# Kernel tuning notes

Hardware: AMD Instinct MI355X
Metric: run time of the kernel (lower is better)

Reference implementation:

```python
import jax, jax.numpy as jnp
import numpy as np

D_MODEL = 256
N_LAYER = 8
N_HEAD = 8
D_K = D_MODEL // N_HEAD  # 32
D_FF = 4 * D_MODEL
VOCAB = 5
NUM_BUCKETS = 64
MAX_DIST = 256
L = 768
B = 1
EPS = 1e-5


def _ln(x, s, b):
    m = jnp.mean(x, axis=-1, keepdims=True)
    v = jnp.mean((x - m) ** 2, axis=-1, keepdims=True)
    return (x - m) * jax.lax.rsqrt(v + EPS) * s + b


def _rp_bucket(rel_pos):
    # faithful to RelativePositionBias._relative_position_bucket
    nb = NUM_BUCKETS // 2  # 32
    ret = (rel_pos < 0).astype(jnp.int32) * nb
    arp = jnp.abs(rel_pos)
    max_exact = nb // 2  # 16
    is_small = arp < max_exact
    safe = jnp.maximum(arp, 1).astype(jnp.float32)
    log_ratio = float(np.log(MAX_DIST / max_exact))
    vil = max_exact + (jnp.log(safe / max_exact) / log_ratio * (nb - max_exact)).astype(jnp.int32)
    vil = jnp.minimum(vil, nb - 1)
    return ret + jnp.where(is_small, arp.astype(jnp.int32), vil)


def setup_inputs() -> dict:
    key = jax.random.key(0)
    ks = iter(jax.random.split(key, 40))
    s = 0.02
    d = {}
    d['seq'] = jax.random.randint(next(ks), (B, L), 0, VOCAB, dtype=jnp.int32)
    d['tok_emb'] = jax.random.normal(next(ks), (VOCAB, D_MODEL), jnp.float32) * s
    d['rp_emb'] = jax.random.normal(next(ks), (NUM_BUCKETS, N_HEAD), jnp.float32) * s
    # stacked per-layer params [N_LAYER, ...]
    d['wq'] = jax.random.normal(next(ks), (N_LAYER, D_MODEL, D_MODEL), jnp.float32) * s
    d['wk'] = jax.random.normal(next(ks), (N_LAYER, D_MODEL, D_MODEL), jnp.float32) * s
    d['wv'] = jax.random.normal(next(ks), (N_LAYER, D_MODEL, D_MODEL), jnp.float32) * s
    d['wo'] = jax.random.normal(next(ks), (N_LAYER, D_MODEL, D_MODEL), jnp.float32) * s
    d['ln1_s'] = jnp.ones((N_LAYER, D_MODEL), jnp.float32)
    d['ln1_b'] = jnp.zeros((N_LAYER, D_MODEL), jnp.float32)
    d['ln2_s'] = jnp.ones((N_LAYER, D_MODEL), jnp.float32)
    d['ln2_b'] = jnp.zeros((N_LAYER, D_MODEL), jnp.float32)
    d['ffn_w1'] = jax.random.normal(next(ks), (N_LAYER, D_MODEL, D_FF), jnp.float32) * s
    d['ffn_b1'] = jnp.zeros((N_LAYER, D_FF), jnp.float32)
    d['ffn_w2'] = jax.random.normal(next(ks), (N_LAYER, D_FF, D_MODEL), jnp.float32) * s
    d['ffn_b2'] = jnp.zeros((N_LAYER, D_MODEL), jnp.float32)
    d['lnf_s'] = jnp.ones((D_MODEL,), jnp.float32)
    d['lnf_b'] = jnp.zeros((D_MODEL,), jnp.float32)
    d['pair_q_w'] = jax.random.normal(next(ks), (D_MODEL, D_MODEL), jnp.float32) * s
    d['pair_q_b'] = jnp.zeros((D_MODEL,), jnp.float32)
    d['pair_k_w'] = jax.random.normal(next(ks), (D_MODEL, D_MODEL), jnp.float32) * s
    d['pair_k_b'] = jnp.zeros((D_MODEL,), jnp.float32)
    d['pair_rp_emb'] = jax.random.normal(next(ks), (NUM_BUCKETS, D_MODEL), jnp.float32) * s
    d['cls_w1'] = jax.random.normal(next(ks), (D_MODEL, D_MODEL), jnp.float32) * s
    d['cls_b1'] = jnp.zeros((D_MODEL,), jnp.float32)
    d['cls_w2'] = jax.random.normal(next(ks), (D_MODEL, 2), jnp.float32) * s
    d['cls_b2'] = jnp.zeros((2,), jnp.float32)
    return d


def reference(seq, tok_emb, rp_emb, wq, wk, wv, wo, ln1_s, ln1_b, ln2_s, ln2_b,
              ffn_w1, ffn_b1, ffn_w2, ffn_b2, lnf_s, lnf_b,
              pair_q_w, pair_q_b, pair_k_w, pair_k_b, pair_rp_emb,
              cls_w1, cls_b1, cls_w2, cls_b2):
    scale = D_K ** 0.5
    x = tok_emb[seq]  # [B, L, D]
    pos = jnp.arange(L)
    rel = pos[:, None] - pos[None, :]  # [L, L]
    bucket = _rp_bucket(rel)  # [L, L] int32
    bias = jnp.transpose(rp_emb[bucket], (2, 0, 1))[None]  # [1, H, L, L]

    def step(x, p):
        Wq, Wk, Wv, Wo, s1, b1, s2, b2, fw1, fb1, fw2, fb2 = p
        h = _ln(x, s1, b1)
        q = (h @ Wq).reshape(B, L, N_HEAD, D_K).transpose(0, 2, 1, 3)
        k = (h @ Wk).reshape(B, L, N_HEAD, D_K).transpose(0, 2, 1, 3)
        v = (h @ Wv).reshape(B, L, N_HEAD, D_K).transpose(0, 2, 1, 3)
        attn = jnp.einsum('bhid,bhjd->bhij', q / scale, k) + bias
        attn = jax.nn.softmax(attn, axis=-1)
        o = jnp.einsum('bhij,bhjd->bhid', attn, v)
        o = o.transpose(0, 2, 1, 3).reshape(B, L, D_MODEL) @ Wo
        x = x + o
        h2 = _ln(x, s2, b2)
        f = jax.nn.gelu(h2 @ fw1 + fb1, approximate=False) @ fw2 + fb2
        return x + f, None

    x, _ = jax.lax.scan(step, x, (wq, wk, wv, wo, ln1_s, ln1_b, ln2_s, ln2_b,
                                  ffn_w1, ffn_b1, ffn_w2, ffn_b2))
    x = _ln(x, lnf_s, lnf_b)
    q = x @ pair_q_w + pair_q_b  # [B, L, D]
    k = x @ pair_k_w + pair_k_b
    px = jnp.einsum('bic,bjc->bijc', q, k)  # [B, L, L, D]
    px = px + pair_rp_emb[bucket][None]  # add [L, L, D] pair rel-pos embedding
    px = jax.nn.relu(px @ cls_w1 + cls_b1) @ cls_w2 + cls_b2  # [B, L, L, 2]
    return px
```

## Files before the change

kernel.cpp:

```cpp
#include <hip/hip_runtime.h>
#include <hip/hip_bf16.h>
#include <stdint.h>

#define LSEQ 768
#define DM   256
#define NH   8
#define DK   32
#define DFF  1024
#define NLAYER 8
#define NDD  1535

typedef __attribute__((ext_vector_type(8))) short     bf16x8;
typedef __attribute__((ext_vector_type(8))) _Float16  f16x8;
typedef __attribute__((ext_vector_type(4))) float     f32x4;

__device__ __forceinline__ unsigned short f2bf(float f) {
  unsigned u = __float_as_uint(f);
  u += 0x7fffu + ((u >> 16) & 1u);
  return (unsigned short)(u >> 16);
}
__device__ __forceinline__ unsigned short f2h(float f) {
  union { _Float16 h; unsigned short s; } c;
  c.h = (_Float16)f;
  return c.s;
}
__device__ __forceinline__ int bucket_of(int dd) {
  int rel = dd - 767;
  int ret = rel < 0 ? 32 : 0;
  int arp = rel < 0 ? -rel : rel;
  if (arp < 16) return ret + arp;
  const float lr = 2.772588722239781f;
  float val = logf((float)arp * 0.0625f) / lr * 16.0f;
  int vi = 16 + (int)val;
  return ret + (vi < 31 ? vi : 31);
}

__device__ __forceinline__ void pack8h(unsigned short* dst, int id,
                                       const float* src, int N, int G) {
  int lane = (id >> 3) & 63;
  int rem = id >> 9;
  int g = rem % G, kc = rem / G;
  int kb = kc * 32 + ((lane >> 4) << 3);
  int n = g * 16 + (lane & 15);
  union { unsigned short s[8]; uint4 v; } U;
  #pragma unroll
  for (int e = 0; e < 8; ++e) U.s[e] = f2h(src[(size_t)(kb + e) * N + n]);
  *(uint4*)(dst + id) = U.v;
}

__device__ __forceinline__ void pack8h_cat(unsigned short* dst, int id,
                                           const float* s0, const float* s1,
                                           const float* s2, int G) {
  int lane = (id >> 3) & 63;
  int rem = id >> 9;
  int g = rem % G, kc = rem / G;
  int kb = kc * 32 + ((lane >> 4) << 3);
  int n = g * 16 + (lane & 15);
  const float* sp = n < 256 ? s0 : (n < 512 ? s1 : s2);
  int nn = n & 255;
  union { unsigned short s[8]; uint4 v; } U;
  #pragma unroll
  for (int e = 0; e < 8; ++e) U.s[e] = f2h(sp[(size_t)(kb + e) * 256 + nn]);
  *(uint4*)(dst + id) = U.v;
}

template <int LN, int GR>
__device__ void gemm_tile(const float* gsrc, const int* seqIdx,
                          const float* B, const float* bias, float* C,
                          const float* lns, const float* lnb,
                          int M, int K, int N, int m0, int n0, char* smc) {
  float (*As)[32][68] = (float (*)[32][68])smc;
  float (*Bs)[32][68] = (float (*)[32][68])(smc + 17408);
  float (*stat)[2]    = (float (*)[2])(smc + 34816);
  float (*red)[8]     = (float (*)[8])(smc + 35328);

  int t = threadIdx.x;
  int arow = t >> 2, akq = (t & 3) * 8;
  int mg = m0 + arow;
  int mgc = mg < M ? mg : M - 1;
  const float* Ar = (GR == 1) ? (gsrc + (size_t)seqIdx[mgc] * K)
                              : (gsrc + (size_t)bucket_of(mgc) * K);
  float mean = 0.f, rstd = 0.f;
  if (LN) {
    int lq = t & 3;
    float s = 0.f, s2 = 0.f;
    const float* p = Ar + lq * 64;
    #pragma unroll
    for (int c = 0; c < 64; c += 4) {
      float4 v = *(const float4*)(p + c);
      s  += v.x + v.y + v.z + v.w;
      s2 += v.x * v.x + v.y * v.y + v.z * v.z + v.w * v.w;
    }
    red[arow][lq] = s; red[arow][lq + 4] = s2;
    __syncthreads();
    if (lq == 0) {
      float sm = red[arow][0] + red[arow][1] + red[arow][2] + red[arow][3];
      float sq = red[arow][4] + red[arow][5] + red[arow][6] + red[arow][7];
      float m = sm * (1.f / 256.f);
      float v = sq * (1.f / 256.f) - m * m;
      stat[arow][0] = m;
      stat[arow][1] = rsqrtf(v + 1e-5f);
    }
    __syncthreads();
    mean = stat[arow][0]; rstd = stat[arow][1];
  }

  int bkr = t >> 3, bn8 = (t & 7) * 8;
  int ty = t >> 4, tx = t & 15;
  float acc[4][4] = {};
  int nk = K >> 5;

  for (int kt = 0; kt < nk; ++kt) {
    int k0 = kt << 5;
    float4 a0 = *(const float4*)(Ar + k0 + akq);
    float4 a1 = *(const float4*)(Ar + k0 + akq + 4);
    if (LN) {
      float4 ls0 = *(const float4*)(lns + k0 + akq), ls1 = *(const float4*)(lns + k0 + akq + 4);
      float4 lb0 = *(const float4*)(lnb + k0 + akq), lb1 = *(const float4*)(lnb + k0 + akq + 4);
      a0.x=(a0.x-mean)*rstd*ls0.x+lb0.x; a0.y=(a0.y-mean)*rstd*ls0.y+lb0.y;
      a0.z=(a0.z-mean)*rstd*ls0.z+lb0.z; a0.w=(a0.w-mean)*rstd*ls0.w+lb0.w;
      a1.x=(a1.x-mean)*rstd*ls1.x+lb1.x; a1.y=(a1.y-mean)*rstd*ls1.y+lb1.y;
      a1.z=(a1.z-mean)*rstd*ls1.z+lb1.z; a1.w=(a1.w-mean)*rstd*ls1.w+lb1.w;
    }
    int cur = kt & 1;
    As[cur][akq+0][arow]=a0.x; As[cur][akq+1][arow]=a0.y; As[cur][akq+2][arow]=a0.z; As[cur][akq+3][arow]=a0.w;
    As[cur][akq+4][arow]=a1.x; As[cur][akq+5][arow]=a1.y; As[cur][akq+6][arow]=a1.z; As[cur][akq+7][arow]=a1.w;
    *(float4*)&Bs[cur][bkr][bn8] = *(const float4*)(B + (size_t)(k0 + bkr) * N + n0 + bn8);
    *(float4*)&Bs[cur][bkr][bn8+4] = *(const float4*)(B + (size_t)(k0 + bkr) * N + n0 + bn8 + 4);
    __syncthreads();
    #pragma unroll 8
    for (int kk = 0; kk < 32; ++kk) {
      float4 a = *(float4*)&As[cur][kk][ty * 4];
      float4 b = *(float4*)&Bs[cur][kk][tx * 4];
      acc[0][0]=fmaf(a.x,b.x,acc[0][0]); acc[0][1]=fmaf(a.x,b.y,acc[0][1]);
      acc[0][2]=fmaf(a.x,b.z,acc[0][2]); acc[0][3]=fmaf(a.x,b.w,acc[0][3]);
      acc[1][0]=fmaf(a.y,b.x,acc[1][0]); acc[1][1]=fmaf(a.y,b.y,acc[1][1]);
      acc[1][2]=fmaf(a.y,b.z,acc[1][2]); acc[1][3]=fmaf(a.y,b.w,acc[1][3]);
      acc[2][0]=fmaf(a.z,b.x,acc[2][0]); acc[2][1]=fmaf(a.z,b.y,acc[2][1]);
      acc[2][2]=fmaf(a.z,b.z,acc[2][2]); acc[2][3]=fmaf(a.z,b.w,acc[2][3]);
      acc[3][0]=fmaf(a.w,b.x,acc[3][0]); acc[3][1]=fmaf(a.w,b.y,acc[3][1]);
      acc[3][2]=fmaf(a.w,b.z,acc[3][2]); acc[3][3]=fmaf(a.w,b.w,acc[3][3]);
    }
    __syncthreads();
  }

  #pragma unroll
  for (int u = 0; u < 4; ++u) {
    int m = m0 + ty * 4 + u;
    if (m < M) {
      int n = n0 + tx * 4;
      float4 val = make_float4(acc[u][0], acc[u][1], acc[u][2], acc[u][3]);
      if (bias) {
        float4 bv = *(const float4*)(bias + n);
        val.x += bv.x; val.y += bv.y; val.z += bv.z; val.w += bv.w;
      }
      *(float4*)(C + (size_t)m * N + n) = val;
    }
  }
}

__global__ __launch_bounds__(256, 2) void k_prep(
    const int* __restrict__ seq, const float* __restrict__ tok_emb,
    const float* __restrict__ rp_emb,
    const float* __restrict__ wq, const float* __restrict__ wk,
    const float* __restrict__ wv, const float* __restrict__ wo,
    const float* __restrict__ ffn_w1, const float* __restrict__ ffn_w2,
    const float* __restrict__ ln1s0, const float* __restrict__ ln1b0,
    const float* __restrict__ pair_rp, const float* __restrict__ cls_w1,
    const float* __restrict__ cls_b1,
    const float* __restrict__ pair_q_w, const float* __restrict__ pair_k_w,
    float* x0, float* q0, float* k0, float* v0, float* RB,
    unsigned short* W1p, float* abias,
    unsigned short* Wop, unsigned short* W1pk, unsigned short* W2pk,
    unsigned short* Wqkvp, unsigned short* Wpairp) {
  __shared__ __align__(16) char sm[37376];
  int b = blockIdx.x, t = threadIdx.x;
  if (b < 96) {
    int m0 = (b % 24) * 64, n0 = (b / 24) * 64;
    gemm_tile<0,2>(pair_rp, nullptr, cls_w1, cls_b1, RB,
                   nullptr, nullptr, NDD, 256, 256, m0, n0, sm);
  } else if (b < 240) {
    int u = b - 96;
    int n0g = (u % 12) * 64, m0 = (u / 12) * 64;
    int bi = n0g >> 8, n0 = n0g & 255;
    const float* B = bi == 0 ? wq : (bi == 1 ? wk : wv);
    float* C = bi == 0 ? q0 : (bi == 1 ? k0 : v0);
    gemm_tile<1,1>(tok_emb, seq, B, nullptr, C,
                   ln1s0, ln1b0, LSEQ, 256, 256, m0, n0, sm);
  } else if (b < 432) {
    int row = (b - 240) * 4 + (t >> 6), c = (t & 63) * 4;
    *(float4*)(x0 + (size_t)row * DM + c) =
        *(const float4*)(tok_emb + (size_t)seq[row] * DM + c);
  } else if (b < 438) {
    int dd = (b - 432) * 256 + t;
    if (dd < NDD) {
      int bk = bucket_of(dd);
      #pragma unroll
      for (int h = 0; h < NH; ++h) abias[dd * 8 + h] = rp_emb[bk * 8 + h];
    }
  } else if (b < 502) {
    int base = (b - 438) * 1024 + t * 4;
    #pragma unroll
    for (int uu = 0; uu < 4; ++uu) {
      int id = base + uu;
      int e = id & 7, lane = (id >> 3) & 63, g = (id >> 9) & 15, kc = id >> 13;
      int kg = kc * 32 + (lane >> 4) * 8 + e;
      int n  = g * 16 + (lane & 15);
      W1p[id] = f2h(cls_w1[(size_t)kg * 256 + n]);
    }
  } else {
    int u = (b - 502) * 2048 + t * 8;
    if (u < 524288) {
      int layer = u >> 16, id = u & 65535;
      pack8h(Wop + ((size_t)layer << 16), id, wo + ((size_t)layer << 16), 256, 16);
    } else if (u < 2621440) {
      int v2 = u - 524288; int layer = v2 >> 18, id = v2 & 262143;
      pack8h(W1pk + ((size_t)layer << 18), id, ffn_w1 + ((size_t)layer << 18), 1024, 64);
    } else if (u < 4718592) {
      int v2 = u - 2621440; int layer = v2 >> 18, id = v2 & 262143;
      pack8h(W2pk + ((size_t)layer << 18), id, ffn_w2 + ((size_t)layer << 18), 256, 16);
    } else if (u < 6291456) {
      int v2 = u - 4718592; int layer = v2 / 196608, id = v2 - layer * 196608;
      pack8h_cat(Wqkvp + (size_t)layer * 196608, id,
                 wq + ((size_t)layer << 16), wk + ((size_t)layer << 16),
                 wv + ((size_t)layer << 16), 48);
    } else {
      int id = u - 6291456;
      pack8h_cat(Wpairp, id, pair_q_w, pair_k_w, pair_k_w, 32);
    }
  }
}

#define ATTN_SMEM 72960

__global__ __launch_bounds__(256, 2) void k_attn2(
    const float* __restrict__ q, const float* __restrict__ k,
    const float* __restrict__ v, const float* __restrict__ abias,
    float* __restrict__ o) {
  extern __shared__ char sm[];
  float* S  = (float*)sm;
  float* KV = (float*)(sm + 49664);
  float* QS = (float*)(sm + 66560);
  float* BS = (float*)(sm + 68672);
  float (*red)[16] = (float (*)[16])(sm + 71808);
  float* mrow = (float*)(sm + 72832);
  float* linv = (float*)(sm + 72896);

  int i0 = blockIdx.x * 16, h = blockIdx.y, hc = h * DK;
  int t = threadIdx.x;

  for (int u = t; u < 783; u += 256)
    BS[u] = abias[(size_t)(i0 + u) * 8 + h];
  {
    int r = t >> 4, c = t & 15;
    const float inv = 0.17677669529663687f;
    QS[r * 33 + c]      = q[(size_t)(i0 + r) * DM + hc + c] * inv;
    QS[r * 33 + c + 16] = q[(size_t)(i0 + r) * DM + hc + c + 16] * inv;
  }

  int kx = t & 31, ry = t >> 5;
  int key = t >> 1, half = t & 1;

  for (int cc = 0; cc < 6; ++cc) {
    const float* kp = k + (size_t)(cc * 128 + key) * DM + hc + half * 16;
    float4 L0 = *(const float4*)(kp);
    float4 L1 = *(const float4*)(kp + 4);
    float4 L2 = *(const float4*)(kp + 8);
    float4 L3 = *(const float4*)(kp + 12);
    __syncthreads();
    int cb = half * 16;
    KV[(cb+ 0)*132+key]=L0.x; KV[(cb+ 1)*132+key]=L0.y; KV[(cb+ 2)*132+key]=L0.z; KV[(cb+ 3)*132+key]=L0.w;
    KV[(cb+ 4)*132+key]=L1.x; KV[(cb+ 5)*132+key]=L1.y; KV[(cb+ 6)*132+key]=L1.z; KV[(cb+ 7)*132+key]=L1.w;
    KV[(cb+ 8)*132+key]=L2.x; KV[(cb+ 9)*132+key]=L2.y; KV[(cb+10)*132+key]=L2.z; KV[(cb+11)*132+key]=L2.w;
    KV[(cb+12)*132+key]=L3.x; KV[(cb+13)*132+key]=L3.y; KV[(cb+14)*132+key]=L3.z; KV[(cb+15)*132+key]=L3.w;
    __syncthreads();

    float s0x=0,s0y=0,s0z=0,s0w=0, s1x=0,s1y=0,s1z=0,s1w=0;
    #pragma unroll
    for (int kk = 0; kk < 32; ++kk) {
      float q0 = QS[(ry*2    )*33 + kk];
      float q1 = QS[(ry*2 + 1)*33 + kk];
      float4 kv4 = *(const float4*)&KV[kk*132 + kx*4];
      s0x = fmaf(q0, kv4.x, s0x); s0y = fmaf(q0, kv4.y, s0y);
      s0z = fmaf(q0, kv4.z, s0z); s0w = fmaf(q0, kv4.w, s0w);
      s1x = fmaf(q1, kv4.x, s1x); s1y = fmaf(q1, kv4.y, s1y);
      s1z = fmaf(q1, kv4.z, s1z); s1w = fmaf(q1, kv4.w, s1w);
    }
    int jb = cc * 128 + kx * 4;
    int r0 = ry * 2, r1 = r0 + 1;
    S[r0*776 + jb+0] = s0x + BS[r0 + 767 - (jb+0)];
    S[r0*776 + jb+1] = s0y + BS[r0 + 767 - (jb+1)];
    S[r0*776 + jb+2] = s0z + BS[r0 + 767 - (jb+2)];
    S[r0*776 + jb+3] = s0w + BS[r0 + 767 - (jb+3)];
    S[r1*776 + jb+0] = s1x + BS[r1 + 767 - (jb+0)];
    S[r1*776 + jb+1] = s1y + BS[r1 + 767 - (jb+1)];
    S[r1*776 + jb+2] = s1z + BS[r1 + 767 - (jb+2)];
    S[r1*776 + jb+3] = s1w + BS[r1 + 767 - (jb+3)];
  }
  __syncthreads();

  {
    int ti = t >> 4, tj = t & 15;
    float mx = -1e30f;
    for (int jc = 0; jc < 48; ++jc)
      mx = fmaxf(mx, S[ti*776 + jc*16 + tj]);
    red[ti][tj] = mx;
    __syncthreads();
    if (tj == 0) {
      float m2 = red[ti][0];
      #pragma unroll
      for (int u = 1; u < 16; ++u) m2 = fmaxf(m2, red[ti][u]);
      mrow[ti] = m2;
    }
    __syncthreads();
    float m2 = mrow[ti];
    float sum = 0.f;
    for (int jc = 0; jc < 48; ++jc) {
      int j = jc*16 + tj;
      float e = __expf(S[ti*776 + j] - m2);
      S[ti*776 + j] = e;
      sum += e;
    }
    red[ti][tj] = sum;
    __syncthreads();
    if (tj == 0) {
      float s2 = 0.f;
      #pragma unroll
      for (int u = 0; u < 16; ++u) s2 += red[ti][u];
      linv[ti] = 1.f / s2;
    }
  }

  int cp = t & 15, jg = t >> 4;
  int c0 = cp * 2, c1 = c0 + 1;
  float oc0[16] = {}, oc1[16] = {};
  for (int cc = 0; cc < 6; ++cc) {
    const float* vp = v + (size_t)(cc * 128 + key) * DM + hc + half * 16;
    float4 L0 = *(const float4*)(vp);
    float4 L1 = *(const float4*)(vp + 4);
    float4 L2 = *(const float4*)(vp + 8);
    float4 L3 = *(const float4*)(vp + 12);
    __syncthreads();
    int cb = half * 16;
    KV[(cb+ 0)*132+key]=L0.x; KV[(cb+ 1)*132+key]=L0.y; KV[(cb+ 2)*132+key]=L0.z; KV[(cb+ 3)*132+key]=L0.w;
    KV[(cb+ 4)*132+key]=L1.x; KV[(cb+ 5)*132+key]=L1.y; KV[(cb+ 6)*132+key]=L1.z; KV[(cb+ 7)*132+key]=L1.w;
    KV[(cb+ 8)*132+key]=L2.x; KV[(cb+ 9)*132+key]=L2.y; KV[(cb+10)*132+key]=L2.z; KV[(cb+11)*132+key]=L2.w;
    KV[(cb+12)*132+key]=L3.x; KV[(cb+13)*132+key]=L3.y; KV[(cb+14)*132+key]=L3.z; KV[(cb+15)*132+key]=L3.w;
    __syncthreads();

    #pragma unroll
    for (int jj2 = 0; jj2 < 2; ++jj2) {
      int jb = jg * 8 + jj2 * 4;
      float4 vA = *(const float4*)&KV[c0*132 + jb];
      float4 vB = *(const float4*)&KV[c1*132 + jb];
      #pragma unroll
      for (int r = 0; r < 16; ++r) {
        float4 sv = *(const float4*)&S[r*776 + cc*128 + jb];
        oc0[r] += sv.x*vA.x + sv.y*vA.y + sv.z*vA.z + sv.w*vA.w;
        oc1[r] += sv.x*vB.x + sv.y*vB.y + sv.z*vB.z + sv.w*vB.w;
      }
    }
  }

  #pragma unroll
  for (int h2 = 0; h2 < 2; ++h2) {
    __syncthreads();
    #pragma unroll
    for (int r = 0; r < 8; ++r) {
      KV[(jg*8 + r)*32 + c0] = oc0[h2*8 + r];
      KV[(jg*8 + r)*32 + c1] = oc1[h2*8 + r];
    }
    __syncthreads();
    int r = t >> 5, c = t & 31;
    float s = 0.f;
    #pragma unroll
    for (int jgg = 0; jgg < 16; ++jgg) s += KV[(jgg*8 + r)*32 + c];
    o[(size_t)(i0 + h2*8 + r) * DM + hc + c] = s * linv[h2*8 + r];
  }
}


__global__ __launch_bounds__(256, 2) void k_t1(
    const float* __restrict__ o, const float* __restrict__ xin,
    const unsigned short* __restrict__ wop,
    const float* __restrict__ ln2s, const float* __restrict__ ln2b,
    const unsigned short* __restrict__ w1p, const float* __restrict__ fb1,
    float* __restrict__ x1, unsigned short* __restrict__ Fg) {
  __shared__ __align__(16) float    Xf[16][260];
  __shared__ __align__(16) _Float16 Ab[16][264];
  int t = threadIdx.x;
  int i0 = blockIdx.x * 16;
  int by = blockIdx.y;
  int w = t >> 6, l = t & 63;
  int lr = l & 15, lq = l >> 4;

  {
    int r = t >> 4, j = t & 15;
    #pragma unroll
    for (int q = 0; q < 4; ++q) {
      int c = j * 4 + q * 64;
      float4 v = *(const float4*)(o + (size_t)(i0 + r) * DM + c);
      union { _Float16 h[4]; uint2 u; } cv;
      cv.h[0] = (_Float16)v.x; cv.h[1] = (_Float16)v.y;
      cv.h[2] = (_Float16)v.z; cv.h[3] = (_Float16)v.w;
      *(uint2*)&Ab[r][c] = cv.u;
      *(float4*)&Xf[r][c] = *(const float4*)(xin + (size_t)(i0 + r) * DM + c);
    }
  }
  __syncthreads();

  f16x8 af[8];
  #pragma unroll
  for (int kc = 0; kc < 8; ++kc)
    af[kc] = *(const f16x8*)&Ab[lr][kc * 32 + lq * 8];

  {
    const unsigned short* wp = wop + (size_t)l * 8;
    #pragma unroll
    for (int gi = 0; gi < 4; ++gi) {
      int g = w * 4 + gi;
      f32x4 ac = {0.f, 0.f, 0.f, 0.f};
      #pragma unroll
      for (int kc = 0; kc < 8; ++kc) {
        f16x8 bb = *(const f16x8*)(wp + ((kc * 16 + g) << 9));
        ac = __builtin_amdgcn_mfma_f32_16x16x32_f16(af[kc], bb, ac, 0, 0, 0);
      }
      int n = g * 16 + lr;
      #pragma unroll
      for (int r = 0; r < 4; ++r)
        Xf[lq * 4 + r][n] += ac[r];
    }
  }
  __syncthreads();

  if (by == 0) {
    int r = t >> 4, j = t & 15;
    #pragma unroll
    for (int q = 0; q < 4; ++q) {
      int c = j * 4 + q * 64;
      *(float4*)(x1 + (size_t)(i0 + r) * DM + c) = *(const float4*)&Xf[r][c];
    }
  }

  {
    int r = t >> 4, j = t & 15;
    int c0 = j * 16;
    float xv[16]; float s1 = 0.f, s2 = 0.f;
    #pragma unroll
    for (int u = 0; u < 16; ++u) {
      xv[u] = Xf[r][c0 + u];
      s1 += xv[u]; s2 += xv[u] * xv[u];
    }
    #pragma unroll
    for (int m = 1; m < 16; m <<= 1) {
      s1 += __shfl_xor(s1, m);
      s2 += __shfl_xor(s2, m);
    }
    float mean = s1 * (1.f / 256.f);
    float var  = s2 * (1.f / 256.f) - mean * mean;
    float rs = rsqrtf(var + 1e-5f);
    #pragma unroll
    for (int p = 0; p < 4; ++p) {
      union { _Float16 h[4]; uint2 u; } cv;
      #pragma unroll
      for (int e = 0; e < 4; ++e) {
        int c = c0 + p * 4 + e;
        cv.h[e] = (_Float16)((xv[p * 4 + e] - mean) * rs * ln2s[c] + ln2b[c]);
      }
      *(uint2*)&Ab[r][c0 + p * 4] = cv.u;
    }
  }
  __syncthreads();

  #pragma unroll
  for (int kc = 0; kc < 8; ++kc)
    af[kc] = *(const f16x8*)&Ab[lr][kc * 32 + lq * 8];

  {
    const unsigned short* wp = w1p + (size_t)l * 8;
    #pragma unroll
    for (int gi = 0; gi < 4; ++gi) {
      int g = by * 16 + w * 4 + gi;
      f32x4 ac = {0.f, 0.f, 0.f, 0.f};
      #pragma unroll
      for (int kc = 0; kc < 8; ++kc) {
        f16x8 bb = *(const f16x8*)(wp + ((kc * 64 + g) << 9));
        ac = __builtin_amdgcn_mfma_f32_16x16x32_f16(af[kc], bb, ac, 0, 0, 0);
      }
      int n = g * 16 + lr;
      float b1 = fb1[n];
      #pragma unroll
      for (int r = 0; r < 4; ++r) {
        float v = ac[r] + b1;
        v = 0.5f * v * (1.f + erff(v * 0.70710678118654752f));
        Fg[(size_t)(i0 + lq * 4 + r) * DFF + n] = f2h(v);
      }
    }
  }
}

__global__ __launch_bounds__(256, 2) void k_t2(
    const unsigned short* __restrict__ Fg, const float* __restrict__ x1,
    const unsigned short* __restrict__ w2p, const float* __restrict__ fb2,
    float* __restrict__ x2) {
  __shared__ __align__(16) _Float16 Fs[16][1032];
  int t = threadIdx.x;
  int i0 = blockIdx.x * 16;
  int by = blockIdx.y;
  int w = t >> 6, l = t & 63;
  int lr = l & 15, lq = l >> 4;

  {
    int r = t >> 4, j = t & 15;
    #pragma unroll
    for (int q = 0; q < 8; ++q) {
      int c = j * 8 + q * 128;
      *(uint4*)&Fs[r][c] = *(const uint4*)(Fg + (size_t)(i0 + r) * DFF + c);
    }
  }
  __syncthreads();

  int g = by * 4 + w;
  const unsigned short* wp = w2p + (size_t)l * 8;
  f32x4 ac0 = {0.f, 0.f, 0.f, 0.f}, ac1 = {0.f, 0.f, 0.f, 0.f};
  #pragma unroll
  for (int kc = 0; kc < 32; kc += 2) {
    f16x8 fa0 = *(const f16x8*)&Fs[lr][kc * 32 + lq * 8];
    f16x8 bb0 = *(const f16x8*)(wp + ((kc * 16 + g) << 9));
    ac0 = __builtin_amdgcn_mfma_f32_16x16x32_f16(fa0, bb0, ac0, 0, 0, 0);
    f16x8 fa1 = *(const f16x8*)&Fs[lr][(kc + 1) * 32 + lq * 8];
    f16x8 bb1 = *(const f16x8*)(wp + (((kc + 1) * 16 + g) << 9));
    ac1 = __builtin_amdgcn_mfma_f32_16x16x32_f16(fa1, bb1, ac1, 0, 0, 0);
  }
  int n = g * 16 + lr;
  float b2v = fb2[n];
  #pragma unroll
  for (int r = 0; r < 4; ++r) {
    int row = i0 + lq * 4 + r;
    x2[(size_t)row * DM + n] =
        x1[(size_t)row * DM + n] + ac0[r] + ac1[r] + b2v;
  }
}

template <int LAST>
__global__ __launch_bounds__(256, 2) void k_t3(
    const float* __restrict__ x2,
    const float* __restrict__ lns, const float* __restrict__ lnb,
    const unsigned short* __restrict__ wnp,
    const float* __restrict__ nb0, const float* __restrict__ nb1,
    float* __restrict__ qo, float* __restrict__ ko, float* __restrict__ vo) {
  __shared__ __align__(16) _Float16 Ab[16][264];
  int t = threadIdx.x;
  int i0 = blockIdx.x * 16;
  int by = blockIdx.y;
  int w = t >> 6, l = t & 63;
  int lr = l & 15, lq = l >> 4;

  {
    int r = t >> 4, j = t & 15;
    int c0 = j * 16;
    const float* xp = x2 + (size_t)(i0 + r) * DM + c0;
    float xv[16]; float s1 = 0.f, s2 = 0.f;
    #pragma unroll
    for (int u = 0; u < 16; u += 4) {
      float4 v = *(const float4*)(xp + u);
      xv[u] = v.x; xv[u+1] = v.y; xv[u+2] = v.z; xv[u+3] = v.w;
      s1 += v.x + v.y + v.z + v.w;
      s2 += v.x*v.x + v.y*v.y + v.z*v.z + v.w*v.w;
    }
    #pragma unroll
    for (int m = 1; m < 16; m <<= 1) {
      s1 += __shfl_xor(s1, m);
      s2 += __shfl_xor(s2, m);
    }
    float mean = s1 * (1.f / 256.f);
    float var  = s2 * (1.f / 256.f) - mean * mean;
    float rs = rsqrtf(var + 1e-5f);
    #pragma unroll
    for (int p = 0; p < 4; ++p) {
      union { _Float16 h[4]; uint2 u; } cv;
      #pragma unroll
      for (int e = 0; e < 4; ++e) {
        int c = c0 + p * 4 + e;
        cv.h[e] = (_Float16)((xv[p * 4 + e] - mean) * rs * lns[c] + lnb[c]);
      }
      *(uint2*)&Ab[r][c0 + p * 4] = cv.u;
    }
  }
  __syncthreads();

  f16x8 af[8];
  #pragma unroll
  for (int kc = 0; kc < 8; ++kc)
    af[kc] = *(const f16x8*)&Ab[lr][kc * 32 + lq * 8];

  const unsigned short* wp = wnp + (size_t)l * 8;
  if (!LAST) {
    #pragma unroll
    for (int gi = 0; gi < 3; ++gi) {
      int g = by * 12 + w * 3 + gi;
      f32x4 ac = {0.f, 0.f, 0.f, 0.f};
      #pragma unroll
      for (int kc = 0; kc < 8; ++kc) {
        f16x8 bb = *(const f16x8*)(wp + ((kc * 48 + g) << 9));
        ac = __builtin_amdgcn_mfma_f32_16x16x32_f16(af[kc], bb, ac, 0, 0, 0);
      }
      int n = g * 16 + lr;
      float* dst = n < 256 ? qo : (n < 512 ? ko : vo);
      int nn = n & 255;
      #pragma unroll
      for (int r = 0; r < 4; ++r)
        dst[(size_t)(i0 + lq * 4 + r) * DM + nn] = ac[r];
    }
  } else {
    #pragma unroll
    for (int gi = 0; gi < 2; ++gi) {
      int g = by * 8 + w * 2 + gi;
      f32x4 ac = {0.f, 0.f, 0.f, 0.f};
      #pragma unroll
      for (int kc = 0; kc < 8; ++kc) {
        f16x8 bb = *(const f16x8*)(wp + ((kc * 32 + g) << 9));
        ac = __builtin_amdgcn_mfma_f32_16x16x32_f16(af[kc], bb, ac, 0, 0, 0);
      }
      int n = g * 16 + lr;
      float* dst = n < 256 ? qo : ko;
      const float* bias = n < 256 ? nb0 : nb1;
      int nn = n & 255;
      float bv = bias[nn];
      #pragma unroll
      for (int r = 0; r < 4; ++r)
        dst[(size_t)(i0 + lq * 4 + r) * DM + nn] = ac[r] + bv;
    }
  }
}

__global__ __launch_bounds__(256, 2) void k_pair3(
    const float* __restrict__ pq, const float* __restrict__ pk,
    const unsigned short* __restrict__ W1p, const float* __restrict__ RB,
    const float* __restrict__ w2, const float* __restrict__ b2,
    float* __restrict__ out) {
  __shared__ __align__(16) _Float16 qsh[4][264];
  __shared__ __align__(16) _Float16 ksh[32][264];
  __shared__ __align__(16) float    RB_s[35][260];
  __shared__ float racc[256];

  int t = threadIdx.x;
  int j0 = blockIdx.x * 32;
  int i0 = blockIdx.y * 4;
  int w = t >> 6, l = t & 63;
  int q4 = l >> 4, l15 = l & 15;
  int mwv = w & 1, nwv = w >> 1;

  {
    if (t < 128) {
      int kr = t >> 5, c8 = (t & 31) * 8;
      const float* sp = pq + (size_t)(i0 + kr) * DM + c8;
      float4 a = *(const float4*)sp, b = *(const float4*)(sp + 4);
      f16x8 h;
      h[0]=(_Float16)a.x; h[1]=(_Float16)a.y; h[2]=(_Float16)a.z; h[3]=(_Float16)a.w;
      h[4]=(_Float16)b.x; h[5]=(_Float16)b.y; h[6]=(_Float16)b.z; h[7]=(_Float16)b.w;
      *(f16x8*)&qsh[kr][c8] = h;
    }
    #pragma unroll
    for (int r8 = 0; r8 < 4; ++r8) {
      int idx = t + r8 * 256;
      int kr = idx >> 5, c8 = (idx & 31) * 8;
      const float* sp = pk + (size_t)(j0 + kr) * DM + c8;
      float4 a = *(const float4*)sp, b = *(const float4*)(sp + 4);
      f16x8 h;
      h[0]=(_Float16)a.x; h[1]=(_Float16)a.y; h[2]=(_Float16)a.z; h[3]=(_Float16)a.w;
      h[4]=(_Float16)b.x; h[5]=(_Float16)b.y; h[6]=(_Float16)b.z; h[7]=(_Float16)b.w;
      *(f16x8*)&ksh[kr][c8] = h;
    }
    int ddmin = i0 - j0 + 736;
    for (int idx = t; idx < 35 * 64; idx += 256) {
      int lc = idx >> 6, c4b = (idx & 63) * 4;
      *(float4*)&RB_s[lc][c4b] =
          *(const float4*)(RB + (size_t)(ddmin + lc) * 256 + c4b);
    }
    racc[t] = 0.f;
  }
  __syncthreads();

  const unsigned short* Bp = W1p + (size_t)(nwv * 8) * 512 + (size_t)l * 8;

  f32x4 acc[4][8];
  #pragma unroll
  for (int aa = 0; aa < 4; ++aa)
    #pragma unroll
    for (int bb = 0; bb < 8; ++bb) acc[aa][bb] = (f32x4){0.f, 0.f, 0.f, 0.f};

  f16x8 bcur[8];
  #pragma unroll
  for (int nt = 0; nt < 8; ++nt) bcur[nt] = *(const f16x8*)(Bp + nt * 512);

  for (int kc = 0; kc < 8; ++kc) {
    f16x8 bnxt[8];
    if (kc < 7) {
      const unsigned short* bbn = Bp + (size_t)(kc + 1) * 8192;
      #pragma unroll
      for (int nt = 0; nt < 8; ++nt) bnxt[nt] = *(const f16x8*)(bbn + nt * 512);
    }
    int c = kc * 32 + q4 * 8;
    f16x8 qa = *(const f16x8*)&qsh[mwv * 2][c];
    f16x8 qb = *(const f16x8*)&qsh[mwv * 2 + 1][c];
    f16x8 ka = *(const f16x8*)&ksh[l15][c];
    f16x8 kb = *(const f16x8*)&ksh[16 + l15][c];

    f16x8 af0 = qa * ka;
    f16x8 af1 = qa * kb;
    f16x8 af2 = qb * ka;
    f16x8 af3 = qb * kb;

    #pragma unroll
    for (int nt = 0; nt < 8; ++nt) {
      acc[0][nt] = __builtin_amdgcn_mfma_f32_16x16x32_f16(af0, bcur[nt], acc[0][nt], 0, 0, 0);
      acc[1][nt] = __builtin_amdgcn_mfma_f32_16x16x32_f16(af1, bcur[nt], acc[1][nt], 0, 0, 0);
      acc[2][nt] = __builtin_amdgcn_mfma_f32_16x16x32_f16(af2, bcur[nt], acc[2][nt], 0, 0, 0);
      acc[3][nt] = __builtin_amdgcn_mfma_f32_16x16x32_f16(af3, bcur[nt], acc[3][nt], 0, 0, 0);
    }
    if (kc < 7) {
      #pragma unroll
      for (int nt = 0; nt < 8; ++nt) bcur[nt] = bnxt[nt];
    }
  }

  float w20[8], w21[8];
  #pragma unroll
  for (int nt = 0; nt < 8; ++nt) {
    int n = nwv * 128 + nt * 16 + l15;
    w20[nt] = w2[n * 2];
    w21[nt] = w2[n * 2 + 1];
  }
  #pragma unroll
  for (int mt = 0; mt < 4; ++mt) {
    #pragma unroll
    for (int reg = 0; reg < 4; ++reg) {
      int r = mwv * 64 + mt * 16 + q4 * 4 + reg;
      int lc = (r >> 5) - (r & 31) + 31;
      float o0 = 0.f, o1 = 0.f;
      #pragma unroll
      for (int nt = 0; nt < 8; ++nt) {
        int n = nwv * 128 + nt * 16 + l15;
        float T = acc[mt][nt][reg] + RB_s[lc][n];
        T = fmaxf(T, 0.f);
        o0 = fmaf(T, w20[nt], o0);
        o1 = fmaf(T, w21[nt], o1);
      }
      #pragma unroll
      for (int s = 1; s < 16; s <<= 1) {
        o0 += __shfl_xor(o0, s);
        o1 += __shfl_xor(o1, s);
      }
      if (l15 == 0) {
        atomicAdd(&racc[r * 2 + 0], o0);
        atomicAdd(&racc[r * 2 + 1], o1);
      }
    }
  }
  __syncthreads();
  {
    int r = t >> 1, oo = t & 1;
    out[((size_t)(i0 + (r >> 5)) * LSEQ + (j0 + (r & 31))) * 2 + oo] = racc[t] + b2[oo];
  }
}

extern "C" void kernel_launch(void* const* d_in, const int* in_sizes, int n_in,
                              void* d_out, int out_size, void* d_ws, size_t ws_size,
                              hipStream_t stream) {
  const int*   seq      = (const int*)  d_in[0];
  const float* tok_emb  = (const float*)d_in[1];
  const float* rp_emb   = (const float*)d_in[2];
  const float* wq       = (const float*)d_in[3];
  const float* wk       = (const float*)d_in[4];
  const float* wv       = (const float*)d_in[5];
  const float* wo       = (const float*)d_in[6];
  const float* ln1_s    = (const float*)d_in[7];
  const float* ln1_b    = (const float*)d_in[8];
  const float* ln2_s    = (const float*)d_in[9];
  const float* ln2_b    = (const float*)d_in[10];
  const float* ffn_w1   = (const float*)d_in[11];
  const float* ffn_b1   = (const float*)d_in[12];
  const float* ffn_w2   = (const float*)d_in[13];
  const float* ffn_b2   = (const float*)d_in[14];
  const float* lnf_s    = (const float*)d_in[15];
  const float* lnf_b    = (const float*)d_in[16];
  const float* pair_q_w = (const float*)d_in[17];
  const float* pair_q_b = (const float*)d_in[18];
  const float* pair_k_w = (const float*)d_in[19];
  const float* pair_k_b = (const float*)d_in[20];
  const float* pair_rp  = (const float*)d_in[21];
  const float* cls_w1   = (const float*)d_in[22];
  const float* cls_b1   = (const float*)d_in[23];
  const float* cls_w2   = (const float*)d_in[24];
  const float* cls_b2   = (const float*)d_in[25];
  float* out = (float*)d_out;

  char* ws = (char*)d_ws;
  float* xb0 = (float*)(ws + 0);
  float* xb1 = (float*)(ws + 786432);
  float* qb[2] = { (float*)(ws + 1572864), (float*)(ws + 3932160) };
  float* kb[2] = { (float*)(ws + 2359296), (float*)(ws + 4718592) };
  float* vb[2] = { (float*)(ws + 3145728), (float*)(ws + 5505024) };
  float* o   = (float*)(ws + 6291456);
  float* pq  = (float*)(ws + 7077888);
  float* pk  = (float*)(ws + 7864320);
  float* RB  = (float*)(ws + 8650752);
  unsigned short* W1p = (unsigned short*)(ws + 10223616);
  float* abias = (float*)(ws + 10354688);
  unsigned short* Wop    = (unsigned short*)(ws + 10403840);
  unsigned short* W1pk   = (unsigned short*)(ws + 11452416);
  unsigned short* W2pk   = (unsigned short*)(ws + 15646720);
  unsigned short* Wqkvp  = (unsigned short*)(ws + 19841024);
  unsigned short* Wpairp = (unsigned short*)(ws + 22986752);
  unsigned short* Fg     = (unsigned short*)(ws + 23248896);
  float* x1buf           = (float*)(ws + 24821760);

  (void)in_sizes; (void)n_in; (void)out_size; (void)ws_size;

  hipFuncSetAttribute(reinterpret_cast<const void*>(k_attn2),
                      hipFuncAttributeMaxDynamicSharedMemorySize, ATTN_SMEM);

  k_prep<<<3638, 256, 0, stream>>>(seq, tok_emb, rp_emb, wq, wk, wv, wo,
                                   ffn_w1, ffn_w2, ln1_s, ln1_b,
                                   pair_rp, cls_w1, cls_b1, pair_q_w, pair_k_w,
                                   xb0, qb[0], kb[0], vb[0], RB, W1p, abias,
                                   Wop, W1pk, W2pk, Wqkvp, Wpairp);

  for (int l = 0; l < NLAYER; ++l) {
    int pi = l & 1, po = pi ^ 1;
    float* xin  = (l & 1) ? xb1 : xb0;
    float* xout = (l & 1) ? xb0 : xb1;

    k_attn2<<<dim3(48, 8), 256, ATTN_SMEM, stream>>>(qb[pi], kb[pi], vb[pi], abias, o);

    k_t1<<<dim3(48, 4), 256, 0, stream>>>(
        o, xin, Wop + ((size_t)l << 16),
        ln2_s + l * DM, ln2_b + l * DM,
        W1pk + ((size_t)l << 18), ffn_b1 + (size_t)l * DFF,
        x1buf, Fg);

    k_t2<<<dim3(48, 4), 256, 0, stream>>>(
        Fg, x1buf, W2pk + ((size_t)l << 18), ffn_b2 + (size_t)l * DM, xout);

    if (l < NLAYER - 1) {
      k_t3<0><<<dim3(48, 4), 256, 0, stream>>>(
          xout, ln1_s + (l + 1) * DM, ln1_b + (l + 1) * DM,
          Wqkvp + (size_t)(l + 1) * 196608, nullptr, nullptr,
          qb[po], kb[po], vb[po]);
    } else {
      k_t3<1><<<dim3(48, 4), 256, 0, stream>>>(
          xout, lnf_s, lnf_b, Wpairp, pair_q_b, pair_k_b,
          pq, pk, nullptr);
    }
  }

  k_pair3<<<dim3(24, 192), 256, 0, stream>>>(pq, pk, W1p, RB, cls_w2, cls_b2, out);
}
```

Baseline: 645.3 us.

## Split Wo/FFN1 kernel and widen grids for more parallelism per layer

Splits the fused Wo-projection + LN2 + FFN1 kernel into separate k_wo and k_ffn1 kernels. Each warp now computes a single 16-column output tile, and the grids grow from 192 blocks to 768 (ffn1, ffn2) or 576/384 (qkv). FFN2 splits its K dimension across the four warps and reduces the partials through shared memory. The aim is to fill more CUs on this small L=768 problem, at the cost of an extra launch per layer, redundant LN2 and A-tile work in every y-block, and an x1 round trip through global memory.

New measurement: 615.4 us. 4.6% less time.

```diff
diff --git a/kernel.cpp b/kernel.cpp
--- a/kernel.cpp
+++ b/kernel.cpp
@@ -380,13 +380,9 @@
 }
 
 
-__global__ __launch_bounds__(256, 2) void k_t1(
+__global__ __launch_bounds__(256, 2) void k_wo(
     const float* __restrict__ o, const float* __restrict__ xin,
-    const unsigned short* __restrict__ wop,
-    const float* __restrict__ ln2s, const float* __restrict__ ln2b,
-    const unsigned short* __restrict__ w1p, const float* __restrict__ fb1,
-    float* __restrict__ x1, unsigned short* __restrict__ Fg) {
-  __shared__ __align__(16) float    Xf[16][260];
+    const unsigned short* __restrict__ wop, float* __restrict__ x1) {
   __shared__ __align__(16) _Float16 Ab[16][264];
   int t = threadIdx.x;
   int i0 = blockIdx.x * 16;
@@ -404,7 +400,6 @@
       cv.h[0] = (_Float16)v.x; cv.h[1] = (_Float16)v.y;
       cv.h[2] = (_Float16)v.z; cv.h[3] = (_Float16)v.w;
       *(uint2*)&Ab[r][c] = cv.u;
-      *(float4*)&Xf[r][c] = *(const float4*)(xin + (size_t)(i0 + r) * DM + c);
     }
   }
   __syncthreads();
@@ -414,42 +409,45 @@
   for (int kc = 0; kc < 8; ++kc)
     af[kc] = *(const f16x8*)&Ab[lr][kc * 32 + lq * 8];
 
-  {
-    const unsigned short* wp = wop + (size_t)l * 8;
-    #pragma unroll
-    for (int gi = 0; gi < 4; ++gi) {
-      int g = w * 4 + gi;
-      f32x4 ac = {0.f, 0.f, 0.f, 0.f};
-      #pragma unroll
-      for (int kc = 0; kc < 8; ++kc) {
-        f16x8 bb = *(const f16x8*)(wp + ((kc * 16 + g) << 9));
-        ac = __builtin_amdgcn_mfma_f32_16x16x32_f16(af[kc], bb, ac, 0, 0, 0);
-      }
-      int n = g * 16 + lr;
-      #pragma unroll
-      for (int r = 0; r < 4; ++r)
-        Xf[lq * 4 + r][n] += ac[r];
-    }
-  }
-  __syncthreads();
-
-  if (by == 0) {
-    int r = t >> 4, j = t & 15;
-    #pragma unroll
-    for (int q = 0; q < 4; ++q) {
-      int c = j * 4 + q * 64;
-      *(float4*)(x1 + (size_t)(i0 + r) * DM + c) = *(const float4*)&Xf[r][c];
-    }
-  }
+  int g = by * 4 + w;
+  const unsigned short* wp = wop + (size_t)l * 8;
+  f32x4 ac = {0.f, 0.f, 0.f, 0.f};
+  #pragma unroll
+  for (int kc = 0; kc < 8; ++kc) {
+    f16x8 bb = *(const f16x8*)(wp + ((kc * 16 + g) << 9));
+    ac = __builtin_amdgcn_mfma_f32_16x16x32_f16(af[kc], bb, ac, 0, 0, 0);
+  }
+  int n = g * 16 + lr;
+  #pragma unroll
+  for (int r = 0; r < 4; ++r) {
+    int row = i0 + lq * 4 + r;
+    x1[(size_t)row * DM + n] = xin[(size_t)row * DM + n] + ac[r];
+  }
+}
+
+__global__ __launch_bounds__(256, 2) void k_ffn1(
+    const float* __restrict__ x1,
+    const float* __restrict__ ln2s, const float* __restrict__ ln2b,
+    const unsigned short* __restrict__ w1p, const float* __restrict__ fb1,
+    unsigned short* __restrict__ Fg) {
+  __shared__ __align__(16) _Float16 Ab[16][264];
+  int t = threadIdx.x;
+  int i0 = blockIdx.x * 16;
+  int by = blockIdx.y;
+  int w = t >> 6, l = t & 63;
+  int lr = l & 15, lq = l >> 4;
 
   {
     int r = t >> 4, j = t & 15;
     int c0 = j * 16;
+    const float* xp = x1 + (size_t)(i0 + r) * DM + c0;
     float xv[16]; float s1 = 0.f, s2 = 0.f;
     #pragma unroll
-    for (int u = 0; u < 16; ++u) {
-      xv[u] = Xf[r][c0 + u];
-      s1 += xv[u]; s2 += xv[u] * xv[u];
+    for (int u = 0; u < 16; u += 4) {
+      float4 v = *(const float4*)(xp + u);
+      xv[u] = v.x; xv[u+1] = v.y; xv[u+2] = v.z; xv[u+3] = v.w;
+      s1 += v.x + v.y + v.z + v.w;
+      s2 += v.x*v.x + v.y*v.y + v.z*v.z + v.w*v.w;
     }
     #pragma unroll
     for (int m = 1; m < 16; m <<= 1) {
@@ -472,41 +470,38 @@
   }
   __syncthreads();
 
+  f16x8 af[8];
   #pragma unroll
   for (int kc = 0; kc < 8; ++kc)
     af[kc] = *(const f16x8*)&Ab[lr][kc * 32 + lq * 8];
 
-  {
-    const unsigned short* wp = w1p + (size_t)l * 8;
-    #pragma unroll
-    for (int gi = 0; gi < 4; ++gi) {
-      int g = by * 16 + w * 4 + gi;
-      f32x4 ac = {0.f, 0.f, 0.f, 0.f};
-      #pragma unroll
-      for (int kc = 0; kc < 8; ++kc) {
-        f16x8 bb = *(const f16x8*)(wp + ((kc * 64 + g) << 9));
-        ac = __builtin_amdgcn_mfma_f32_16x16x32_f16(af[kc], bb, ac, 0, 0, 0);
-      }
-      int n = g * 16 + lr;
-      float b1 = fb1[n];
-      #pragma unroll
-      for (int r = 0; r < 4; ++r) {
-        float v = ac[r] + b1;
-        v = 0.5f * v * (1.f + erff(v * 0.70710678118654752f));
-        Fg[(size_t)(i0 + lq * 4 + r) * DFF + n] = f2h(v);
-      }
-    }
-  }
-}
-
-__global__ __launch_bounds__(256, 2) void k_t2(
+  int g = by * 4 + w;
+  const unsigned short* wp = w1p + (size_t)l * 8;
+  f32x4 ac = {0.f, 0.f, 0.f, 0.f};
+  #pragma unroll
+  for (int kc = 0; kc < 8; ++kc) {
+    f16x8 bb = *(const f16x8*)(wp + ((kc * 64 + g) << 9));
+    ac = __builtin_amdgcn_mfma_f32_16x16x32_f16(af[kc], bb, ac, 0, 0, 0);
+  }
+  int n = g * 16 + lr;
+  float b1 = fb1[n];
+  #pragma unroll
+  for (int r = 0; r < 4; ++r) {
+    float v = ac[r] + b1;
+    v = 0.5f * v * (1.f + erff(v * 0.70710678118654752f));
+    Fg[(size_t)(i0 + lq * 4 + r) * DFF + n] = f2h(v);
+  }
+}
+
+__global__ __launch_bounds__(256, 2) void k_ffn2(
     const unsigned short* __restrict__ Fg, const float* __restrict__ x1,
     const unsigned short* __restrict__ w2p, const float* __restrict__ fb2,
     float* __restrict__ x2) {
   __shared__ __align__(16) _Float16 Fs[16][1032];
+  __shared__ float part[3][16][17];
   int t = threadIdx.x;
   int i0 = blockIdx.x * 16;
-  int by = blockIdx.y;
+  int g = blockIdx.y;
   int w = t >> 6, l = t & 63;
   int lr = l & 15, lq = l >> 4;
 
@@ -520,25 +515,31 @@
   }
   __syncthreads();
 
-  int g = by * 4 + w;
   const unsigned short* wp = w2p + (size_t)l * 8;
-  f32x4 ac0 = {0.f, 0.f, 0.f, 0.f}, ac1 = {0.f, 0.f, 0.f, 0.f};
-  #pragma unroll
-  for (int kc = 0; kc < 32; kc += 2) {
-    f16x8 fa0 = *(const f16x8*)&Fs[lr][kc * 32 + lq * 8];
-    f16x8 bb0 = *(const f16x8*)(wp + ((kc * 16 + g) << 9));
-    ac0 = __builtin_amdgcn_mfma_f32_16x16x32_f16(fa0, bb0, ac0, 0, 0, 0);
-    f16x8 fa1 = *(const f16x8*)&Fs[lr][(kc + 1) * 32 + lq * 8];
-    f16x8 bb1 = *(const f16x8*)(wp + (((kc + 1) * 16 + g) << 9));
-    ac1 = __builtin_amdgcn_mfma_f32_16x16x32_f16(fa1, bb1, ac1, 0, 0, 0);
-  }
-  int n = g * 16 + lr;
-  float b2v = fb2[n];
-  #pragma unroll
-  for (int r = 0; r < 4; ++r) {
-    int row = i0 + lq * 4 + r;
-    x2[(size_t)row * DM + n] =
-        x1[(size_t)row * DM + n] + ac0[r] + ac1[r] + b2v;
+  f32x4 ac = {0.f, 0.f, 0.f, 0.f};
+  #pragma unroll
+  for (int k8 = 0; k8 < 8; ++k8) {
+    int kc = w * 8 + k8;
+    f16x8 fa = *(const f16x8*)&Fs[lr][kc * 32 + lq * 8];
+    f16x8 bb = *(const f16x8*)(wp + ((kc * 16 + g) << 9));
+    ac = __builtin_amdgcn_mfma_f32_16x16x32_f16(fa, bb, ac, 0, 0, 0);
+  }
+  if (w > 0) {
+    #pragma unroll
+    for (int r = 0; r < 4; ++r)
+      part[w - 1][lq * 4 + r][lr] = ac[r];
+  }
+  __syncthreads();
+  if (w == 0) {
+    int n = g * 16 + lr;
+    float b2v = fb2[n];
+    #pragma unroll
+    for (int r = 0; r < 4; ++r) {
+      int rr = lq * 4 + r;
+      int row = i0 + rr;
+      float s = ac[r] + part[0][rr][lr] + part[1][rr][lr] + part[2][rr][lr];
+      x2[(size_t)row * DM + n] = x1[(size_t)row * DM + n] + s + b2v;
+    }
   }
 }
 
@@ -595,42 +596,35 @@
     af[kc] = *(const f16x8*)&Ab[lr][kc * 32 + lq * 8];
 
   const unsigned short* wp = wnp + (size_t)l * 8;
+  int g = by * 4 + w;
   if (!LAST) {
-    #pragma unroll
-    for (int gi = 0; gi < 3; ++gi) {
-      int g = by * 12 + w * 3 + gi;
-      f32x4 ac = {0.f, 0.f, 0.f, 0.f};
-      #pragma unroll
-      for (int kc = 0; kc < 8; ++kc) {
-        f16x8 bb = *(const f16x8*)(wp + ((kc * 48 + g) << 9));
-        ac = __builtin_amdgcn_mfma_f32_16x16x32_f16(af[kc], bb, ac, 0, 0, 0);
-      }
-      int n = g * 16 + lr;
-      float* dst = n < 256 ? qo : (n < 512 ? ko : vo);
-      int nn = n & 255;
-      #pragma unroll
-      for (int r = 0; r < 4; ++r)
-        dst[(size_t)(i0 + lq * 4 + r) * DM + nn] = ac[r];
-    }
+    f32x4 ac = {0.f, 0.f, 0.f, 0.f};
+    #pragma unroll
+    for (int kc = 0; kc < 8; ++kc) {
+      f16x8 bb = *(const f16x8*)(wp + ((kc * 48 + g) << 9));
+      ac = __builtin_amdgcn_mfma_f32_16x16x32_f16(af[kc], bb, ac, 0, 0, 0);
+    }
+    int n = g * 16 + lr;
+    float* dst = n < 256 ? qo : (n < 512 ? ko : vo);
+    int nn = n & 255;
+    #pragma unroll
+    for (int r = 0; r < 4; ++r)
+      dst[(size_t)(i0 + lq * 4 + r) * DM + nn] = ac[r];
   } else {
-    #pragma unroll
-    for (int gi = 0; gi < 2; ++gi) {
-      int g = by * 8 + w * 2 + gi;
-      f32x4 ac = {0.f, 0.f, 0.f, 0.f};
-      #pragma unroll
-      for (int kc = 0; kc < 8; ++kc) {
-        f16x8 bb = *(const f16x8*)(wp + ((kc * 32 + g) << 9));
-        ac = __builtin_amdgcn_mfma_f32_16x16x32_f16(af[kc], bb, ac, 0, 0, 0);
-      }
-      int n = g * 16 + lr;
-      float* dst = n < 256 ? qo : ko;
-      const float* bias = n < 256 ? nb0 : nb1;
-      int nn = n & 255;
-      float bv = bias[nn];
-      #pragma unroll
-      for (int r = 0; r < 4; ++r)
-        dst[(size_t)(i0 + lq * 4 + r) * DM + nn] = ac[r] + bv;
-    }
+    f32x4 ac = {0.f, 0.f, 0.f, 0.f};
+    #pragma unroll
+    for (int kc = 0; kc < 8; ++kc) {
+      f16x8 bb = *(const f16x8*)(wp + ((kc * 32 + g) << 9));
+      ac = __builtin_amdgcn_mfma_f32_16x16x32_f16(af[kc], bb, ac, 0, 0, 0);
+    }
+    int n = g * 16 + lr;
+    float* dst = n < 256 ? qo : ko;
+    const float* bias = n < 256 ? nb0 : nb1;
+    int nn = n & 255;
+    float bv = bias[nn];
+    #pragma unroll
+    for (int r = 0; r < 4; ++r)
+      dst[(size_t)(i0 + lq * 4 + r) * DM + nn] = ac[r] + bv;
   }
 }
 
@@ -834,22 +828,22 @@
 
     k_attn2<<<dim3(48, 8), 256, ATTN_SMEM, stream>>>(qb[pi], kb[pi], vb[pi], abias, o);
 
-    k_t1<<<dim3(48, 4), 256, 0, stream>>>(
-        o, xin, Wop + ((size_t)l << 16),
-        ln2_s + l * DM, ln2_b + l * DM,
-        W1pk + ((size_t)l << 18), ffn_b1 + (size_t)l * DFF,
-        x1buf, Fg);
-
-    k_t2<<<dim3(48, 4), 256, 0, stream>>>(
+    k_wo<<<dim3(48, 4), 256, 0, stream>>>(o, xin, Wop + ((size_t)l << 16), x1buf);
+
+    k_ffn1<<<dim3(48, 16), 256, 0, stream>>>(
+        x1buf, ln2_s + l * DM, ln2_b + l * DM,
+        W1pk + ((size_t)l << 18), ffn_b1 + (size_t)l * DFF, Fg);
+
+    k_ffn2<<<dim3(48, 16), 256, 0, stream>>>(
         Fg, x1buf, W2pk + ((size_t)l << 18), ffn_b2 + (size_t)l * DM, xout);
 
     if (l < NLAYER - 1) {
-      k_t3<0><<<dim3(48, 4), 256, 0, stream>>>(
+      k_t3<0><<<dim3(48, 12), 256, 0, stream>>>(
           xout, ln1_s + (l + 1) * DM, ln1_b + (l + 1) * DM,
           Wqkvp + (size_t)(l + 1) * 196608, nullptr, nullptr,
           qb[po], kb[po], vb[po]);
     } else {
-      k_t3<1><<<dim3(48, 4), 256, 0, stream>>>(
+      k_t3<1><<<dim3(48, 8), 256, 0, stream>>>(
           xout, lnf_s, lnf_b, Wpairp, pair_q_b, pair_k_b,
           pq, pk, nullptr);
     }
```
